# Performance work log

Measured on AMD Instinct MI355X. Metric: run time of the kernel, lower is better.

The kernel has to match this reference:

```python
import jax, jax.numpy as jnp
import numpy as np

B = 4096          # number of sampled constraints (batch)
H = 1024          # hidden_size
N_UNIT = 5
MAXD = 4          # max(DEPTHS)
TAU = 1.0
N_STEPS = N_UNIT * (1 + 2 * MAXD)  # 45
CLIST = np.linspace(10.0, 20.0, 5).astype(np.float32)
NSC = 11
DEPTH_VALS = np.array([2, 3, 4])
RATIO_VALS = np.array([3, 4, 6])
KS_VALS = np.array([3, 5, 7])


def setup_inputs() -> dict:
    key = jax.random.key(0)
    ks = jax.random.split(key, 20)
    def p(k, shape):
        return jax.random.uniform(k, shape, minval=-0.1, maxval=0.1, dtype=jnp.float32)
    return {
        'constraints': jax.random.uniform(ks[0], (B,), minval=10.0, maxval=20.0, dtype=jnp.float32),
        'superclass_id': 3,
        'gumbel_u': jax.random.uniform(ks[1], (N_STEPS, B, 3), minval=1e-6, maxval=1.0 - 1e-6, dtype=jnp.float32),
        'cond_emb': p(ks[2], (len(CLIST), H // 2)),
        'sc_emb': p(ks[3], (NSC, H // 2)),
        'depth_emb': p(ks[4], (3, H)),
        'ratio_emb': p(ks[5], (3, H)),
        'ks_emb': p(ks[6], (3, H)),
        'W_ih': p(ks[7], (4 * H, H)), 'b_ih': p(ks[8], (4 * H,)),
        'W_hh': p(ks[9], (4 * H, H)), 'b_hh': p(ks[10], (4 * H,)),
        'depth_W': p(ks[11], (3, H)), 'depth_b': p(ks[12], (3,)),
        'width_W': p(ks[13], (3, H)), 'width_b': p(ks[14], (3,)),
        'ks_W': p(ks[15], (3, H)), 'ks_b': p(ks[16], (3,)),
    }


def reference(constraints, superclass_id, gumbel_u, cond_emb, sc_emb, depth_emb, ratio_emb,
              ks_emb, W_ih, b_ih, W_hh, b_hh, depth_W, depth_b, width_W, width_b, ks_W, ks_b):
    clist = jnp.asarray(CLIST)
    # linear_interpolation: find bracketing interval for each constraint
    idx = jnp.clip(jnp.searchsorted(clist, constraints, side='right') - 1, 0, clist.shape[0] - 2)
    left, right = clist[idx], clist[idx + 1]
    w = ((right - constraints) / (right - left))[:, None]
    cemb = w * cond_emb[idx] + (1.0 - w) * cond_emb[idx + 1]          # [B, H/2]
    sce = jnp.broadcast_to(sc_emb[superclass_id], (constraints.shape[0], sc_emb.shape[1]))
    embed = jnp.concatenate([cemb, sce], axis=1)                       # [B, H]
    h = jnp.zeros((constraints.shape[0], H), embed.dtype)
    c = h

    def lstm(x, h, c):
        gates = x @ W_ih.T + b_ih + h @ W_hh.T + b_hh                  # [B, 4H]
        i, f, g, o = jnp.split(gates, 4, axis=-1)
        c2 = jax.nn.sigmoid(f) * c + jax.nn.sigmoid(i) * jnp.tanh(g)
        h2 = jax.nn.sigmoid(o) * jnp.tanh(c2)
        return h2, c2

    def gsample(logits, u):
        g = -jnp.log(-jnp.log(u))
        y_soft = jax.nn.softmax((logits + g) / TAU, axis=-1)
        onehot = jax.nn.one_hot(jnp.argmax(y_soft, -1), logits.shape[-1], dtype=y_soft.dtype)
        y_hard = onehot - jax.lax.stop_gradient(y_soft) + y_soft       # straight-through
        return jnp.argmax(y_hard, -1), y_soft, y_hard

    t = 0
    d_idx, d_probs, d_wbs = [], [], []
    r_idx, r_probs, r_wbs = [], [], []
    k_idx, k_probs, k_wbs = [], [], []
    for _unit in range(N_UNIT):
        h, c = lstm(embed, h, c)
        s, ys, yh = gsample(h @ depth_W.T + depth_b, gumbel_u[t]); t += 1
        d_idx.append(s); d_probs.append(ys); d_wbs.append(yh)
        embed = depth_emb[s]
        for _blk in range(MAXD):
            h, c = lstm(embed, h, c)
            s, ys, yh = gsample(h @ width_W.T + width_b, gumbel_u[t]); t += 1
            r_idx.append(s); r_probs.append(ys); r_wbs.append(yh)
            embed = ratio_emb[s]
            h, c = lstm(embed, h, c)
            s, ys, yh = gsample(h @ ks_W.T + ks_b, gumbel_u[t]); t += 1
            k_idx.append(s); k_probs.append(ys); k_wbs.append(yh)
            embed = ks_emb[s]

    depths = jnp.asarray(DEPTH_VALS)[jnp.stack(d_idx)]   # [5, B]
    ratios = jnp.asarray(RATIO_VALS)[jnp.stack(r_idx)]   # [20, B]
    kss = jnp.asarray(KS_VALS)[jnp.stack(k_idx)]         # [20, B]
    return (depths, ratios, kss,
            jnp.stack(d_wbs), jnp.stack(d_probs),
            jnp.stack(r_wbs), jnp.stack(r_probs),
            jnp.stack(k_wbs), jnp.stack(k_probs))
```

## Files before the change

### kernel.cpp

```cpp
#include <hip/hip_runtime.h>
#include <cmath>

namespace {

typedef _Float16 f16;
typedef f16 f16x8 __attribute__((ext_vector_type(8)));
typedef f16 f16x4 __attribute__((ext_vector_type(4)));
typedef float f32x4 __attribute__((ext_vector_type(4)));

constexpr int B  = 4096;
constexpr int H  = 1024;
constexpr int FH = 4 * H;
constexpr int NSTEPS = 45;
constexpr float INVS = 1.0f / 2048.0f;

__device__ __forceinline__ float sigf(float x) { return 1.0f / (1.0f + expf(-x)); }

struct HL { f16 h, l; };
__device__ __forceinline__ HL split16(float a) {
  float ah = (float)(f16)a;
  if (fabsf(a) < 6.1035156e-5f) ah = 0.0f;
  HL r; r.h = (f16)ah; r.l = (f16)((a - ah) * 2048.0f); return r;
}

__device__ __forceinline__ void async16(f16* lds_dst, const f16* gsrc) {
  __builtin_amdgcn_global_load_lds(
      (const __attribute__((address_space(1))) void*)gsrc,
      (__attribute__((address_space(3))) void*)lds_dst, 16, 0, 0);
}

__global__ void convertW_kernel(const float* __restrict__ W,
                                f16* __restrict__ Whi, f16* __restrict__ Wlo) {
  size_t i = ((size_t)blockIdx.x * 256 + threadIdx.x) * 4;
  float4 v = *(const float4*)(W + i);
  HL a = split16(v.x), b = split16(v.y), c = split16(v.z), d = split16(v.w);
  f16x4 hi = {a.h, b.h, c.h, d.h};
  f16x4 lo = {a.l, b.l, c.l, d.l};
  *(f16x4*)(Whi + i) = hi;
  *(f16x4*)(Wlo + i) = lo;
}

__global__ void precompute_kernel(
    const float* __restrict__ W_ih, const float* __restrict__ b_ih, const float* __restrict__ b_hh,
    const float* __restrict__ depth_emb, const float* __restrict__ ratio_emb, const float* __restrict__ ks_emb,
    const float* __restrict__ cond_emb, const float* __restrict__ sc_emb, const int* __restrict__ sid_p,
    float* __restrict__ tblD, float* __restrict__ tblR, float* __restrict__ tblK,
    float* __restrict__ condp, float* __restrict__ base0) {
  const int w4   = threadIdx.x >> 6;
  const int lane = threadIdx.x & 63;
  const int j    = blockIdx.x * 4 + w4;
  const float* wr = W_ih + (size_t)j * H;
  const int k = lane * 16;
  float4 wv0 = *(const float4*)(wr + k);
  float4 wv1 = *(const float4*)(wr + k + 4);
  float4 wv2 = *(const float4*)(wr + k + 8);
  float4 wv3 = *(const float4*)(wr + k + 12);

  auto dot = [&](const float* e) -> float {
    float4 e0 = *(const float4*)(e);
    float4 e1 = *(const float4*)(e + 4);
    float4 e2 = *(const float4*)(e + 8);
    float4 e3 = *(const float4*)(e + 12);
    return e0.x*wv0.x + e0.y*wv0.y + e0.z*wv0.z + e0.w*wv0.w
         + e1.x*wv1.x + e1.y*wv1.y + e1.z*wv1.z + e1.w*wv1.w
         + e2.x*wv2.x + e2.y*wv2.y + e2.z*wv2.z + e2.w*wv2.w
         + e3.x*wv3.x + e3.y*wv3.y + e3.z*wv3.z + e3.w*wv3.w;
  };

  float a[15];
  a[0] = dot(depth_emb + k);       a[1] = dot(depth_emb + H + k);   a[2] = dot(depth_emb + 2*H + k);
  a[3] = dot(ratio_emb + k);       a[4] = dot(ratio_emb + H + k);   a[5] = dot(ratio_emb + 2*H + k);
  a[6] = dot(ks_emb + k);          a[7] = dot(ks_emb + H + k);      a[8] = dot(ks_emb + 2*H + k);
  a[9] = a[10] = a[11] = a[12] = a[13] = a[14] = 0.0f;
  constexpr int HH = H / 2;
  int sid = sid_p[0];
  if (lane < 32) {
    a[9]  = dot(cond_emb + 0*HH + k);
    a[10] = dot(cond_emb + 1*HH + k);
    a[11] = dot(cond_emb + 2*HH + k);
    a[12] = dot(cond_emb + 3*HH + k);
    a[13] = dot(cond_emb + 4*HH + k);
  } else {
    a[14] = dot(sc_emb + sid*HH + (k - HH));
  }
  #pragma unroll
  for (int i = 0; i < 15; ++i) {
    #pragma unroll
    for (int off = 32; off > 0; off >>= 1) a[i] += __shfl_xor(a[i], off);
  }
  if (lane == 0) {
    float bias = b_ih[j] + b_hh[j];
    tblD[0*FH+j]=a[0]+bias; tblD[1*FH+j]=a[1]+bias; tblD[2*FH+j]=a[2]+bias;
    tblR[0*FH+j]=a[3]+bias; tblR[1*FH+j]=a[4]+bias; tblR[2*FH+j]=a[5]+bias;
    tblK[0*FH+j]=a[6]+bias; tblK[1*FH+j]=a[7]+bias; tblK[2*FH+j]=a[8]+bias;
    condp[0*FH+j]=a[9]; condp[1*FH+j]=a[10]; condp[2*FH+j]=a[11];
    condp[3*FH+j]=a[12]; condp[4*FH+j]=a[13];
    base0[j] = a[14] + bias;
  }
}

__global__ void step0_kernel(const float* __restrict__ constraints,
                             const float* __restrict__ condp, const float* __restrict__ base0,
                             f16* __restrict__ hhi, f16* __restrict__ hlo, float* __restrict__ c) {
  int idx = blockIdx.x * blockDim.x + threadIdx.x;
  int b = idx >> 10;
  int j = idx & (H - 1);
  float cv = constraints[b];
  int i0 = 0;
  if (cv >= 12.5f) i0 = 1;
  if (cv >= 15.0f) i0 = 2;
  if (cv >= 17.5f) i0 = 3;
  float right = 10.0f + 2.5f * (float)(i0 + 1);
  float w = (right - cv) / 2.5f;
  const float* c0 = condp + (size_t)i0 * FH;
  const float* c1 = c0 + FH;
  float iw = 1.0f - w;
  float xi = w*c0[j]       + iw*c1[j]       + base0[j];
  float xg = w*c0[2*H+j]   + iw*c1[2*H+j]   + base0[2*H+j];
  float xo = w*c0[3*H+j]   + iw*c1[3*H+j]   + base0[3*H+j];
  float cn = sigf(xi) * tanhf(xg);
  float hn = sigf(xo) * tanhf(cn);
  c[idx] = cn;
  HL s = split16(hn);
  hhi[idx] = s.h; hlo[idx] = s.l;
}

constexpr int BUFE = 24576;

__device__ __forceinline__ void stage_tile(
    f16* buf, const f16* hhi, const f16* hlo,
    const f16* Whi, const f16* Wlo,
    int b0, int j0, int kt, int tid, int w) {
  int rs = tid >> 2;
  int cs = tid & 3;
  #pragma unroll
  for (int p = 0; p < 2; ++p) {
    int r  = p * 128 + rs;
    int cl = cs ^ (r & 3) ^ ((r >> 2) & 3);
    size_t src = (size_t)(b0 + r) * H + kt + cl * 8;
    f16* dstA = buf + p * 4096 + w * 512;
    async16(dstA, hhi + src);
    async16(dstA + 8192, hlo + src);
  }
  {
    int r  = rs;
    int cl = cs ^ (r & 3) ^ ((r >> 2) & 3);
    int wrow = ((r >> 5) << 10) + j0 + (r & 31);
    size_t src = (size_t)wrow * H + kt + cl * 8;
    f16* dstB = buf + 16384 + w * 512;
    async16(dstB, Whi + src);
    async16(dstB + 4096, Wlo + src);
  }
}

__global__ __launch_bounds__(512, 2) void lstm_step_mfma(
    const f16* __restrict__ hhi, const f16* __restrict__ hlo,
    f16* __restrict__ nhhi, f16* __restrict__ nhlo,
    float* __restrict__ cbuf,
    const f16* __restrict__ Whi, const f16* __restrict__ Wlo,
    const float* __restrict__ tbl, const int* __restrict__ sel) {
  __shared__ __align__(16) f16 lds[2 * BUFE];

  const int tid  = threadIdx.x;
  const int lane = tid & 63;
  const int w    = tid >> 6;
  const int wm   = w >> 1, wn = w & 1;
  const int l15  = lane & 15;
  const int kq   = lane >> 4;

  const int L   = blockIdx.x;
  const int xcd = L & 7, seq = L >> 3;
  const int jb  = (xcd << 2) + (seq & 3);
  const int bb  = seq >> 2;
  const int b0  = bb << 8;
  const int j0  = jb << 5;

  f32x4 accH[4][4] = {};
  f32x4 accL[4][4] = {};

  stage_tile(lds, hhi, hlo, Whi, Wlo, b0, j0, 0, tid, w);
  __syncthreads();

  int cur = 0;
  for (int kt = 0; kt < 32; ++kt) {
    if (kt < 31)
      stage_tile(lds + (cur ^ 1) * BUFE, hhi, hlo, Whi, Wlo, b0, j0, (kt + 1) * 32, tid, w);

    const f16* bufc = lds + cur * BUFE;
    f16x8 ah[4], al[4], bh[4], bl[4];
    #pragma unroll
    for (int mf = 0; mf < 4; ++mf) {
      int R = wm * 64 + mf * 16 + l15;
      int c = kq ^ (R & 3) ^ ((R >> 2) & 3);
      int off = R * 32 + c * 8;
      ah[mf] = *(const f16x8*)(bufc + off);
      al[mf] = *(const f16x8*)(bufc + 8192 + off);
    }
    #pragma unroll
    for (int nf = 0; nf < 4; ++nf) {
      int R = nf * 32 + wn * 16 + l15;
      int c = kq ^ (R & 3) ^ ((R >> 2) & 3);
      int off = R * 32 + c * 8;
      bh[nf] = *(const f16x8*)(bufc + 16384 + off);
      bl[nf] = *(const f16x8*)(bufc + 20480 + off);
    }
    #pragma unroll
    for (int mf = 0; mf < 4; ++mf) {
      #pragma unroll
      for (int nf = 0; nf < 4; ++nf) {
        accH[mf][nf] = __builtin_amdgcn_mfma_f32_16x16x32_f16(ah[mf], bh[nf], accH[mf][nf], 0, 0, 0);
        accL[mf][nf] = __builtin_amdgcn_mfma_f32_16x16x32_f16(ah[mf], bl[nf], accL[mf][nf], 0, 0, 0);
        accL[mf][nf] = __builtin_amdgcn_mfma_f32_16x16x32_f16(al[mf], bh[nf], accL[mf][nf], 0, 0, 0);
      }
    }
    __syncthreads();
    cur ^= 1;
  }

  const int j = j0 + wn * 16 + l15;
  #pragma unroll
  for (int mf = 0; mf < 4; ++mf) {
    #pragma unroll
    for (int r = 0; r < 4; ++r) {
      int b = b0 + wm * 64 + mf * 16 + kq * 4 + r;
      int s = sel[b];
      const float* t = tbl + (size_t)s * FH + j;
      float gi = accH[mf][0][r] + accL[mf][0][r] * INVS + t[0];
      float gf = accH[mf][1][r] + accL[mf][1][r] * INVS + t[H];
      float gg = accH[mf][2][r] + accL[mf][2][r] * INVS + t[2*H];
      float go = accH[mf][3][r] + accL[mf][3][r] * INVS + t[3*H];
      size_t off = (size_t)b * H + j;
      float cp = cbuf[off];
      float cn = sigf(gf) * cp + sigf(gi) * tanhf(gg);
      float hn = sigf(go) * tanhf(cn);
      cbuf[off] = cn;
      HL sp = split16(hn);
      nhhi[off] = sp.h;
      nhlo[off] = sp.l;
    }
  }
}

__global__ void sampler_kernel(const f16* __restrict__ hhi, const f16* __restrict__ hlo,
                               const float* __restrict__ selW, const float* __restrict__ selb,
                               const float* __restrict__ gu,
                               float* __restrict__ val_out, float* __restrict__ wb_out,
                               float* __restrict__ p_out,
                               float v0, float v1, float v2,
                               int* __restrict__ sel) {
  int wave = threadIdx.x >> 6;
  int lane = threadIdx.x & 63;
  int b = blockIdx.x * 4 + wave;
  const f16* hh = hhi + (size_t)b * H;
  const f16* hl = hlo + (size_t)b * H;
  float acc0 = 0, acc1 = 0, acc2 = 0;
  #pragma unroll
  for (int ch = 0; ch < 4; ++ch) {
    int k = ch * 256 + lane * 4;
    f16x4 vh = *(const f16x4*)(hh + k);
    f16x4 vl = *(const f16x4*)(hl + k);
    float x0 = (float)vh[0] + (float)vl[0] * INVS;
    float x1 = (float)vh[1] + (float)vl[1] * INVS;
    float x2 = (float)vh[2] + (float)vl[2] * INVS;
    float x3 = (float)vh[3] + (float)vl[3] * INVS;
    float4 w0 = *(const float4*)(selW + k);
    float4 w1 = *(const float4*)(selW + H + k);
    float4 w2 = *(const float4*)(selW + 2*H + k);
    acc0 += x0*w0.x + x1*w0.y + x2*w0.z + x3*w0.w;
    acc1 += x0*w1.x + x1*w1.y + x2*w1.z + x3*w1.w;
    acc2 += x0*w2.x + x1*w2.y + x2*w2.z + x3*w2.w;
  }
  #pragma unroll
  for (int off = 32; off > 0; off >>= 1) {
    acc0 += __shfl_xor(acc0, off);
    acc1 += __shfl_xor(acc1, off);
    acc2 += __shfl_xor(acc2, off);
  }
  if (lane == 0) {
    float y0 = acc0 + selb[0] - logf(-logf(gu[(size_t)b*3 + 0]));
    float y1 = acc1 + selb[1] - logf(-logf(gu[(size_t)b*3 + 1]));
    float y2 = acc2 + selb[2] - logf(-logf(gu[(size_t)b*3 + 2]));
    int s = 0;
    float best = y0;
    if (y1 > best) { s = 1; best = y1; }
    if (y2 > best) { s = 2; best = y2; }
    float e0 = expf(y0 - best), e1 = expf(y1 - best), e2 = expf(y2 - best);
    float inv = 1.0f / (e0 + e1 + e2);
    float p0 = e0 * inv, p1 = e1 * inv, p2 = e2 * inv;
    val_out[b] = (s == 0) ? v0 : ((s == 1) ? v1 : v2);
    wb_out[(size_t)b*3 + 0] = (s == 0) ? 1.0f : 0.0f;
    wb_out[(size_t)b*3 + 1] = (s == 1) ? 1.0f : 0.0f;
    wb_out[(size_t)b*3 + 2] = (s == 2) ? 1.0f : 0.0f;
    p_out[(size_t)b*3 + 0] = p0;
    p_out[(size_t)b*3 + 1] = p1;
    p_out[(size_t)b*3 + 2] = p2;
    sel[b] = s;
  }
}

}

extern "C" void kernel_launch(void* const* d_in, const int* in_sizes, int n_in,
                              void* d_out, int out_size, void* d_ws, size_t ws_size,
                              hipStream_t stream) {
  (void)in_sizes; (void)n_in; (void)out_size; (void)ws_size;
  const float* constraints = (const float*)d_in[0];
  const int*   sid         = (const int*)d_in[1];
  const float* gumbel      = (const float*)d_in[2];
  const float* cond_emb    = (const float*)d_in[3];
  const float* sc_emb      = (const float*)d_in[4];
  const float* depth_emb   = (const float*)d_in[5];
  const float* ratio_emb   = (const float*)d_in[6];
  const float* ks_emb      = (const float*)d_in[7];
  const float* W_ih        = (const float*)d_in[8];
  const float* b_ih        = (const float*)d_in[9];
  const float* W_hh        = (const float*)d_in[10];
  const float* b_hh        = (const float*)d_in[11];
  const float* depth_W     = (const float*)d_in[12];
  const float* depth_b     = (const float*)d_in[13];
  const float* width_W     = (const float*)d_in[14];
  const float* width_b     = (const float*)d_in[15];
  const float* ks_W        = (const float*)d_in[16];
  const float* ks_b        = (const float*)d_in[17];

  float* out = (float*)d_out;
  float* ws  = (float*)d_ws;

  float* cb    = ws;
  f16*   W16hi = (f16*)(cb + (size_t)B * H);
  f16*   W16lo = W16hi + (size_t)FH * H;
  f16*   hhiA  = W16lo + (size_t)FH * H;
  f16*   hloA  = hhiA + (size_t)B * H;
  f16*   hhiB  = hloA + (size_t)B * H;
  f16*   hloB  = hhiB + (size_t)B * H;
  float* tblD  = (float*)(hloB + (size_t)B * H);
  float* tblR  = tblD + 3 * FH;
  float* tblK  = tblR + 3 * FH;
  float* condp = tblK + 3 * FH;
  float* base0 = condp + 5 * FH;
  int*   sel   = (int*)(base0 + FH);

  convertW_kernel<<<(FH * H / 4) / 256, 256, 0, stream>>>(W_hh, W16hi, W16lo);
  precompute_kernel<<<FH / 4, 256, 0, stream>>>(
      W_ih, b_ih, b_hh, depth_emb, ratio_emb, ks_emb, cond_emb, sc_emb, sid,
      tblD, tblR, tblK, condp, base0);
  step0_kernel<<<(B * H) / 256, 256, 0, stream>>>(constraints, condp, base0, hhiA, hloA, cb);

  const float* selW_arr[3] = {depth_W, width_W, ks_W};
  const float* selb_arr[3] = {depth_b, width_b, ks_b};
  const float vals[3][3]   = {{2.f,3.f,4.f},{3.f,4.f,6.f},{3.f,5.f,7.f}};
  float* tbl_arr[3]        = {tblD, tblR, tblK};

  const size_t DEPTHS = 0,            RATIOS = (size_t)5*B,   KSS    = (size_t)25*B,
               DWBS   = (size_t)45*B, DPROBS = (size_t)60*B,
               RWBS   = (size_t)75*B, RPROBS = (size_t)135*B,
               KWBS   = (size_t)195*B, KPROBS = (size_t)255*B;

  f16* hhi_cur = hhiA; f16* hlo_cur = hloA;
  f16* hhi_nxt = hhiB; f16* hlo_nxt = hloB;
  for (int t = 0; t < NSTEPS; ++t) {
    if (t > 0) {
      int pt = (t - 1) % 9;
      int ptype = (pt == 0) ? 0 : ((pt & 1) ? 1 : 2);
      lstm_step_mfma<<<512, 512, 0, stream>>>(
          hhi_cur, hlo_cur, hhi_nxt, hlo_nxt, cb, W16hi, W16lo, tbl_arr[ptype], sel);
      f16* th = hhi_cur; hhi_cur = hhi_nxt; hhi_nxt = th;
      f16* tl = hlo_cur; hlo_cur = hlo_nxt; hlo_nxt = tl;
    }
    int r = t % 9, u = t / 9;
    int ty, row;
    float *valp, *wbp, *pp;
    if (r == 0)      { ty = 0; row = u;
      valp = out + DEPTHS + (size_t)row*B; wbp = out + DWBS + (size_t)row*B*3; pp = out + DPROBS + (size_t)row*B*3; }
    else if (r & 1)  { ty = 1; row = u*4 + (r-1)/2;
      valp = out + RATIOS + (size_t)row*B; wbp = out + RWBS + (size_t)row*B*3; pp = out + RPROBS + (size_t)row*B*3; }
    else             { ty = 2; row = u*4 + (r-2)/2;
      valp = out + KSS + (size_t)row*B;    wbp = out + KWBS + (size_t)row*B*3; pp = out + KPROBS + (size_t)row*B*3; }
    sampler_kernel<<<B / 4, 256, 0, stream>>>(
        hhi_cur, hlo_cur, selW_arr[ty], selb_arr[ty], gumbel + (size_t)t * B * 3,
        valp, wbp, pp, vals[ty][0], vals[ty][1], vals[ty][2], sel);
  }
}
```

Baseline: 5.207 ms.

## Interleave LDS reads, async staging and MFMA groups with explicit barriers and priority

Splits the per-k-tile work into four phases. Each phase loads one B fragment pair, issues part of the next tile's async global-to-LDS copies, then runs that fragment's MFMA group at raised wave priority, with explicit s_barrier and waitcnt fences between phases. The aim is to overlap global loads and LDS reads with matrix math, and to cut register pressure by holding one B fragment at a time instead of four. In exchange it adds many more barriers per k-tile, which could stall waves.

```diff
diff --git a/kernel.cpp b/kernel.cpp
--- a/kernel.cpp
+++ b/kernel.cpp
@@ -127,31 +127,41 @@
 
 constexpr int BUFE = 24576;
 
-__device__ __forceinline__ void stage_tile(
-    f16* buf, const f16* hhi, const f16* hlo,
-    const f16* Whi, const f16* Wlo,
-    int b0, int j0, int kt, int tid, int w) {
-  int rs = tid >> 2;
-  int cs = tid & 3;
-  #pragma unroll
-  for (int p = 0; p < 2; ++p) {
-    int r  = p * 128 + rs;
-    int cl = cs ^ (r & 3) ^ ((r >> 2) & 3);
-    size_t src = (size_t)(b0 + r) * H + kt + cl * 8;
-    f16* dstA = buf + p * 4096 + w * 512;
-    async16(dstA, hhi + src);
-    async16(dstA + 8192, hlo + src);
-  }
-  {
-    int r  = rs;
-    int cl = cs ^ (r & 3) ^ ((r >> 2) & 3);
-    int wrow = ((r >> 5) << 10) + j0 + (r & 31);
-    size_t src = (size_t)wrow * H + kt + cl * 8;
-    f16* dstB = buf + 16384 + w * 512;
-    async16(dstB, Whi + src);
-    async16(dstB + 4096, Wlo + src);
-  }
-}
+__device__ __forceinline__ void stageA(f16* buf, const f16* hhi, const f16* hlo,
+                                       int b0, int kt, int tid, int w, int p) {
+  int rs = tid >> 2, cs = tid & 3;
+  int r  = p * 128 + rs;
+  int cl = cs ^ (r & 3) ^ ((r >> 2) & 3);
+  size_t src = (size_t)(b0 + r) * H + kt + cl * 8;
+  f16* dstA = buf + p * 4096 + w * 512;
+  async16(dstA, hhi + src);
+  async16(dstA + 8192, hlo + src);
+}
+__device__ __forceinline__ void stageB(f16* buf, const f16* Whi, const f16* Wlo,
+                                       int j0, int kt, int tid, int w) {
+  int rs = tid >> 2, cs = tid & 3;
+  int cl = cs ^ (rs & 3) ^ ((rs >> 2) & 3);
+  int wrow = ((rs >> 5) << 10) + j0 + (rs & 31);
+  size_t src = (size_t)wrow * H + kt + cl * 8;
+  f16* dstB = buf + 16384 + w * 512;
+  async16(dstB, Whi + src);
+  async16(dstB + 4096, Wlo + src);
+}
+
+#define BAR __builtin_amdgcn_s_barrier()
+#define LGKM0 do { asm volatile("s_waitcnt lgkmcnt(0)" ::: "memory"); \
+                   __builtin_amdgcn_sched_barrier(0); } while (0)
+#define READB(P) { int Rb = (P) * 32 + wn * 16 + l15; \
+                   int cb = kq ^ (Rb & 3) ^ ((Rb >> 2) & 3); \
+                   int offb = Rb * 32 + cb * 8; \
+                   bh = *(const f16x8*)(bufc + 16384 + offb); \
+                   bl = *(const f16x8*)(bufc + 20480 + offb); }
+#define MMAG(P) _Pragma("unroll") \
+  for (int mf = 0; mf < 4; ++mf) { \
+    accH[mf][P] = __builtin_amdgcn_mfma_f32_16x16x32_f16(ah[mf], bh, accH[mf][P], 0, 0, 0); \
+    accL[mf][P] = __builtin_amdgcn_mfma_f32_16x16x32_f16(ah[mf], bl, accL[mf][P], 0, 0, 0); \
+    accL[mf][P] = __builtin_amdgcn_mfma_f32_16x16x32_f16(al[mf], bh, accL[mf][P], 0, 0, 0); \
+  }
 
 __global__ __launch_bounds__(512, 2) void lstm_step_mfma(
     const f16* __restrict__ hhi, const f16* __restrict__ hlo,
@@ -178,16 +188,20 @@
   f32x4 accH[4][4] = {};
   f32x4 accL[4][4] = {};
 
-  stage_tile(lds, hhi, hlo, Whi, Wlo, b0, j0, 0, tid, w);
-  __syncthreads();
-
-  int cur = 0;
+  stageA(lds, hhi, hlo, b0, 0, tid, w, 0);
+  stageA(lds, hhi, hlo, b0, 0, tid, w, 1);
+  stageB(lds, Whi, Wlo, j0, 0, tid, w);
+  asm volatile("s_waitcnt vmcnt(0)" ::: "memory");
+  BAR;
+
   for (int kt = 0; kt < 32; ++kt) {
-    if (kt < 31)
-      stage_tile(lds + (cur ^ 1) * BUFE, hhi, hlo, Whi, Wlo, b0, j0, (kt + 1) * 32, tid, w);
-
-    const f16* bufc = lds + cur * BUFE;
-    f16x8 ah[4], al[4], bh[4], bl[4];
+    const f16* bufc = lds + (kt & 1) * BUFE;
+    f16* bufn = lds + ((kt & 1) ^ 1) * BUFE;
+    const bool pre = (kt < 31);
+    const int ktn = (kt + 1) << 5;
+
+    f16x8 ah[4], al[4], bh, bl;
+
     #pragma unroll
     for (int mf = 0; mf < 4; ++mf) {
       int R = wm * 64 + mf * 16 + l15;
@@ -196,25 +210,29 @@
       ah[mf] = *(const f16x8*)(bufc + off);
       al[mf] = *(const f16x8*)(bufc + 8192 + off);
     }
-    #pragma unroll
-    for (int nf = 0; nf < 4; ++nf) {
-      int R = nf * 32 + wn * 16 + l15;
-      int c = kq ^ (R & 3) ^ ((R >> 2) & 3);
-      int off = R * 32 + c * 8;
-      bh[nf] = *(const f16x8*)(bufc + 16384 + off);
-      bl[nf] = *(const f16x8*)(bufc + 20480 + off);
-    }
-    #pragma unroll
-    for (int mf = 0; mf < 4; ++mf) {
-      #pragma unroll
-      for (int nf = 0; nf < 4; ++nf) {
-        accH[mf][nf] = __builtin_amdgcn_mfma_f32_16x16x32_f16(ah[mf], bh[nf], accH[mf][nf], 0, 0, 0);
-        accL[mf][nf] = __builtin_amdgcn_mfma_f32_16x16x32_f16(ah[mf], bl[nf], accL[mf][nf], 0, 0, 0);
-        accL[mf][nf] = __builtin_amdgcn_mfma_f32_16x16x32_f16(al[mf], bh[nf], accL[mf][nf], 0, 0, 0);
-      }
-    }
-    __syncthreads();
-    cur ^= 1;
+    READB(0);
+    if (pre) stageA(bufn, hhi, hlo, b0, ktn, tid, w, 0);
+    BAR; LGKM0;
+    __builtin_amdgcn_s_setprio(1); MMAG(0); __builtin_amdgcn_s_setprio(0);
+    BAR;
+
+    READB(1);
+    if (pre) stageA(bufn, hhi, hlo, b0, ktn, tid, w, 1);
+    BAR; LGKM0;
+    __builtin_amdgcn_s_setprio(1); MMAG(1); __builtin_amdgcn_s_setprio(0);
+    BAR;
+
+    READB(2);
+    if (pre) stageB(bufn, Whi, Wlo, j0, ktn, tid, w);
+    BAR; LGKM0;
+    __builtin_amdgcn_s_setprio(1); MMAG(2); __builtin_amdgcn_s_setprio(0);
+    BAR;
+
+    READB(3);
+    BAR; LGKM0;
+    __builtin_amdgcn_s_setprio(1); MMAG(3); __builtin_amdgcn_s_setprio(0);
+    asm volatile("s_waitcnt vmcnt(0)" ::: "memory");
+    BAR;
   }
 
   const int j = j0 + wn * 16 + l15;
```

Measured after the change: 5.392 ms. 3.5% more time.

## Triple-buffer LDS tiles in LSTM MFMA step with explicit vmcnt waits

Applied to the files above, without the earlier changes.

Replaces the double-buffered LDS staging with a three-stage ring so global-to-LDS async loads run two k-tiles ahead. Synchronisation moves from __syncthreads to partial s_waitcnt vmcnt plus a raw s_barrier, letting the newest tile's loads stay in flight across the barrier. Source pointers and swizzled LDS offsets are precomputed outside the loop, and A fragments are loaded per mf to reduce register pressure. This raises LDS use to 144KB per block at two blocks per CU, which may exceed the per-CU LDS budget and lower occupancy. The hand-written waitcnt also relies on the compiler not reordering other memory operations.

```diff
diff --git a/kernel.cpp b/kernel.cpp
--- a/kernel.cpp
+++ b/kernel.cpp
@@ -127,39 +127,13 @@
 
 constexpr int BUFE = 24576;
 
-__device__ __forceinline__ void stage_tile(
-    f16* buf, const f16* hhi, const f16* hlo,
-    const f16* Whi, const f16* Wlo,
-    int b0, int j0, int kt, int tid, int w) {
-  int rs = tid >> 2;
-  int cs = tid & 3;
-  #pragma unroll
-  for (int p = 0; p < 2; ++p) {
-    int r  = p * 128 + rs;
-    int cl = cs ^ (r & 3) ^ ((r >> 2) & 3);
-    size_t src = (size_t)(b0 + r) * H + kt + cl * 8;
-    f16* dstA = buf + p * 4096 + w * 512;
-    async16(dstA, hhi + src);
-    async16(dstA + 8192, hlo + src);
-  }
-  {
-    int r  = rs;
-    int cl = cs ^ (r & 3) ^ ((r >> 2) & 3);
-    int wrow = ((r >> 5) << 10) + j0 + (r & 31);
-    size_t src = (size_t)wrow * H + kt + cl * 8;
-    f16* dstB = buf + 16384 + w * 512;
-    async16(dstB, Whi + src);
-    async16(dstB + 4096, Wlo + src);
-  }
-}
-
 __global__ __launch_bounds__(512, 2) void lstm_step_mfma(
     const f16* __restrict__ hhi, const f16* __restrict__ hlo,
     f16* __restrict__ nhhi, f16* __restrict__ nhlo,
     float* __restrict__ cbuf,
     const f16* __restrict__ Whi, const f16* __restrict__ Wlo,
     const float* __restrict__ tbl, const int* __restrict__ sel) {
-  __shared__ __align__(16) f16 lds[2 * BUFE];
+  __shared__ __align__(16) f16 lds[3 * BUFE];
 
   const int tid  = threadIdx.x;
   const int lane = tid & 63;
@@ -178,43 +152,74 @@
   f32x4 accH[4][4] = {};
   f32x4 accL[4][4] = {};
 
-  stage_tile(lds, hhi, hlo, Whi, Wlo, b0, j0, 0, tid, w);
-  __syncthreads();
-
-  int cur = 0;
+  int offA[4], offB[4];
+  #pragma unroll
+  for (int mf = 0; mf < 4; ++mf) {
+    int R = wm * 64 + mf * 16 + l15;
+    int c = kq ^ (R & 3) ^ ((R >> 2) & 3);
+    offA[mf] = R * 32 + c * 8;
+  }
+  #pragma unroll
+  for (int nf = 0; nf < 4; ++nf) {
+    int R = nf * 32 + wn * 16 + l15;
+    int c = kq ^ (R & 3) ^ ((R >> 2) & 3);
+    offB[nf] = 16384 + R * 32 + c * 8;
+  }
+
+  const int rs = tid >> 2, cs = tid & 3;
+  const int r1 = 128 + rs;
+  const int cl0 = cs ^ (rs & 3) ^ ((rs >> 2) & 3);
+  const int cl1 = cs ^ (r1 & 3) ^ ((r1 >> 2) & 3);
+  const int wrow = ((rs >> 5) << 10) + j0 + (rs & 31);
+  const f16* sA0h = hhi + (size_t)(b0 + rs) * H + cl0 * 8;
+  const f16* sA0l = hlo + (size_t)(b0 + rs) * H + cl0 * 8;
+  const f16* sA1h = hhi + (size_t)(b0 + r1) * H + cl1 * 8;
+  const f16* sA1l = hlo + (size_t)(b0 + r1) * H + cl1 * 8;
+  const f16* sBh  = Whi + (size_t)wrow * H + cl0 * 8;
+  const f16* sBl  = Wlo + (size_t)wrow * H + cl0 * 8;
+  const int dA0 = w * 512, dA1 = 4096 + w * 512, dB = 16384 + w * 512;
+
+  auto stage6 = [&](f16* buf, int ko) {
+    async16(buf + dA0,        sA0h + ko);
+    async16(buf + dA0 + 8192, sA0l + ko);
+    async16(buf + dA1,        sA1h + ko);
+    async16(buf + dA1 + 8192, sA1l + ko);
+    async16(buf + dB,         sBh + ko);
+    async16(buf + dB + 4096,  sBl + ko);
+  };
+
+  f16 *bA = lds, *bB = lds + BUFE, *bC = lds + 2 * BUFE;
+  stage6(bA, 0);
+  stage6(bB, 32);
+  asm volatile("s_waitcnt vmcnt(6)" ::: "memory");
+  __builtin_amdgcn_s_barrier();
+
   for (int kt = 0; kt < 32; ++kt) {
-    if (kt < 31)
-      stage_tile(lds + (cur ^ 1) * BUFE, hhi, hlo, Whi, Wlo, b0, j0, (kt + 1) * 32, tid, w);
-
-    const f16* bufc = lds + cur * BUFE;
-    f16x8 ah[4], al[4], bh[4], bl[4];
-    #pragma unroll
-    for (int mf = 0; mf < 4; ++mf) {
-      int R = wm * 64 + mf * 16 + l15;
-      int c = kq ^ (R & 3) ^ ((R >> 2) & 3);
-      int off = R * 32 + c * 8;
-      ah[mf] = *(const f16x8*)(bufc + off);
-      al[mf] = *(const f16x8*)(bufc + 8192 + off);
-    }
+    if (kt < 30) stage6(bC, (kt + 2) * 32);
+
+    f16x8 bh[4], bl[4];
     #pragma unroll
     for (int nf = 0; nf < 4; ++nf) {
-      int R = nf * 32 + wn * 16 + l15;
-      int c = kq ^ (R & 3) ^ ((R >> 2) & 3);
-      int off = R * 32 + c * 8;
-      bh[nf] = *(const f16x8*)(bufc + 16384 + off);
-      bl[nf] = *(const f16x8*)(bufc + 20480 + off);
+      bh[nf] = *(const f16x8*)(bA + offB[nf]);
+      bl[nf] = *(const f16x8*)(bA + offB[nf] + 4096);
     }
     #pragma unroll
     for (int mf = 0; mf < 4; ++mf) {
+      f16x8 ah = *(const f16x8*)(bA + offA[mf]);
+      f16x8 al = *(const f16x8*)(bA + offA[mf] + 8192);
       #pragma unroll
       for (int nf = 0; nf < 4; ++nf) {
-        accH[mf][nf] = __builtin_amdgcn_mfma_f32_16x16x32_f16(ah[mf], bh[nf], accH[mf][nf], 0, 0, 0);
-        accL[mf][nf] = __builtin_amdgcn_mfma_f32_16x16x32_f16(ah[mf], bl[nf], accL[mf][nf], 0, 0, 0);
-        accL[mf][nf] = __builtin_amdgcn_mfma_f32_16x16x32_f16(al[mf], bh[nf], accL[mf][nf], 0, 0, 0);
+        accH[mf][nf] = __builtin_amdgcn_mfma_f32_16x16x32_f16(ah, bh[nf], accH[mf][nf], 0, 0, 0);
+        accL[mf][nf] = __builtin_amdgcn_mfma_f32_16x16x32_f16(ah, bl[nf], accL[mf][nf], 0, 0, 0);
+        accL[mf][nf] = __builtin_amdgcn_mfma_f32_16x16x32_f16(al, bh[nf], accL[mf][nf], 0, 0, 0);
       }
     }
-    __syncthreads();
-    cur ^= 1;
+
+    if (kt < 30)       asm volatile("s_waitcnt vmcnt(6)" ::: "memory");
+    else if (kt == 30) asm volatile("s_waitcnt vmcnt(0)" ::: "memory");
+    if (kt < 31) __builtin_amdgcn_s_barrier();
+
+    f16* t = bA; bA = bB; bB = bC; bC = t;
   }
 
   const int j = j0 + wn * 16 + l15;
```

New measurement: 5.417 ms. +4.0%, slower.
